# Optimization experiments

Measured on AMD Instinct MI355X. Metric: run time of the kernel, lower is better.

## Reference

```python
import jax, jax.numpy as jnp
import numpy as np

IN_DIM = 128
OUT_DIM = 128
D_MODEL = IN_DIM // 4        # mamba d_model = 32
D_STATE = 16
D_CONV = 4
EXPAND = 2
D_INNER = EXPAND * D_MODEL   # 64
DT_RANK = (D_MODEL + 15) // 16  # ceil(d_model/16) = 2
N_MIXERS = 3                 # shared + 2 experts (stacked on leading axis)
B, DD, HH, WW = 2, 16, 16, 16


def setup_inputs() -> dict:
    key = jax.random.key(0)
    ks = jax.random.split(key, 12)
    rn = lambda k, s, sc=0.05: jax.random.normal(k, s, dtype=jnp.float32) * sc
    M = N_MIXERS
    return {
        "x": jax.random.normal(ks[0], (B, IN_DIM, DD, HH, WW), dtype=jnp.float32),
        "dataset_id": jax.random.randint(ks[1], (B,), 0, 2),
        "ln_g": jnp.ones((M, IN_DIM), jnp.float32),
        "ln_b": jnp.zeros((M, IN_DIM), jnp.float32),
        "in_w": rn(ks[2], (M, 2 * D_INNER, D_MODEL)),
        "conv_w": rn(ks[3], (M, D_INNER, D_CONV), 0.2),
        "conv_b": rn(ks[4], (M, D_INNER), 0.1),
        "xp_w": rn(ks[5], (M, DT_RANK + 2 * D_STATE, D_INNER)),
        "dt_w": rn(ks[6], (M, D_INNER, DT_RANK), 0.2),
        "dt_b": rn(ks[7], (M, D_INNER), 0.1),
        "A_log": jnp.broadcast_to(jnp.log(jnp.arange(1, D_STATE + 1, dtype=jnp.float32)), (M, D_INNER, D_STATE)) + jnp.zeros((M, D_INNER, D_STATE), jnp.float32),
        "Dp": jnp.ones((M, D_INNER), jnp.float32),
        "out_w": rn(ks[8], (M, D_MODEL, D_INNER)),
        "proj_w": rn(ks[9], (M, OUT_DIM, IN_DIM)),
        "proj_b": jnp.zeros((M, OUT_DIM), jnp.float32),
        "skip": jnp.ones((M,), jnp.float32),
    }


def layernorm(x, g, b, eps=1e-5):
    mu = jnp.mean(x, -1, keepdims=True)
    var = jnp.mean((x - mu) ** 2, -1, keepdims=True)
    return (x - mu) * jax.lax.rsqrt(var + eps) * g + b


def mamba(xp, p):
    # Standard Mamba block: in_proj -> causal depthwise conv1d -> selective scan -> SiLU gate -> out_proj
    # xp: (B, L, d_model)
    Bb, L, _ = xp.shape
    xz = jnp.einsum('bld,ed->ble', xp, p["in_w"])            # (B,L,2*d_inner)
    xi, z = jnp.split(xz, 2, axis=-1)
    conv = jax.lax.conv_general_dilated(xi.transpose(0, 2, 1), p["conv_w"][:, None, :], (1,), [(D_CONV - 1, 0)], feature_group_count=D_INNER)
    xi = jax.nn.silu(conv + p["conv_b"][None, :, None]).transpose(0, 2, 1)  # (B,L,d_inner)
    dbc = jnp.einsum('bld,ed->ble', xi, p["xp_w"])
    dt_low = dbc[..., :DT_RANK]
    Bm = dbc[..., DT_RANK:DT_RANK + D_STATE]
    Cm = dbc[..., DT_RANK + D_STATE:]
    delta = jax.nn.softplus(jnp.einsum('blr,dr->bld', dt_low, p["dt_w"]) + p["dt_b"])  # (B,L,d_inner)
    A = -jnp.exp(p["A_log"])                                  # (d_inner, d_state)

    def step(h, inp):
        xt, dt, Bt, Ct = inp                                  # (B,di),(B,di),(B,ds),(B,ds)
        dA = jnp.exp(dt[..., None] * A)                       # (B,d_inner,d_state)
        h = dA * h + (dt * xt)[..., None] * Bt[:, None, :]
        return h, jnp.einsum('bds,bs->bd', h, Ct)

    h0 = jnp.zeros((Bb, D_INNER, D_STATE), xp.dtype)
    xs = (xi.transpose(1, 0, 2), delta.transpose(1, 0, 2), Bm.transpose(1, 0, 2), Cm.transpose(1, 0, 2))
    _, ys = jax.lax.scan(step, h0, xs)
    y = ys.transpose(1, 0, 2) + p["Dp"] * xi
    y = y * jax.nn.silu(z)
    return jnp.einsum('ble,de->bld', y, p["out_w"])


def mixer(x, p):
    # PetaloMixer pom_module='full': LN -> 4-way channel chunk -> shared Mamba + skip -> concat -> LN -> Linear
    Bb, C, Dd, Hh, Ww = x.shape
    L = Dd * Hh * Ww
    xf = x.reshape(Bb, C, L).transpose(0, 2, 1)               # (B,L,C)
    xn = layernorm(xf, p["ln_g"], p["ln_b"])
    parts = jnp.stack(jnp.split(xn, 4, axis=-1), 0)           # (4,B,L,d_model)
    outs = jax.vmap(lambda q: mamba(q, p))(parts) + p["skip"] * parts
    xm = jnp.concatenate([outs[i] for i in range(4)], -1)     # (B,L,C)
    xm = layernorm(xm, p["ln_g"], p["ln_b"])                  # same LayerNorm reused, as in torch code
    xpj = jnp.einsum('blc,oc->blo', xm, p["proj_w"]) + p["proj_b"]
    return xpj.transpose(0, 2, 1).reshape(Bb, OUT_DIM, Dd, Hh, Ww)


def _forward(x, dataset_id, params):
    shared = mixer(x, {k: v[0] for k, v in params.items()})
    # experts: compute both over full batch (vectorized), then per-sample select by dataset_id
    eouts = jax.vmap(lambda p: mixer(x, p))({k: v[1:] for k, v in params.items()})  # (2,B,out,D,H,W)
    ids = jnp.minimum(dataset_id, N_MIXERS - 2)               # clamp: min(m, n_experts-1)
    expert_out = eouts[ids, jnp.arange(x.shape[0])]
    return shared + expert_out                                # Dropout3d(p=0.2) is identity in eval mode


def reference(x, dataset_id, ln_g, ln_b, in_w, conv_w, conv_b, xp_w, dt_w, dt_b, A_log, Dp, out_w, proj_w, proj_b, skip):
    params = dict(ln_g=ln_g, ln_b=ln_b, in_w=in_w, conv_w=conv_w, conv_b=conv_b, xp_w=xp_w, dt_w=dt_w, dt_b=dt_b, A_log=A_log, Dp=Dp, out_w=out_w, proj_w=proj_w, proj_b=proj_b, skip=skip)
    return _forward(x, dataset_id, params)
```

## Files before the change

### kernel.cpp

```cpp
#include <hip/hip_runtime.h>
#include <math.h>

#define LSEQ 4096
#define CIN  128
#define DI   64
#define NS   16
#define NP   4
#define NJ   4
#define NSEQ 16
#define NC   128
#define LC   32
#define LOG2E 1.44269504f
#define LN2   0.6931471806f

__device__ __forceinline__ int mixer_of(const int* did, int j){
  if((j&1)==0) return 0;
  int d = did[j>>1];
  return 1 + (d < 1 ? d : 1);
}
__device__ __forceinline__ float fexp2(float x){ return __builtin_amdgcn_exp2f(x); }
__device__ __forceinline__ float silu_f(float x){
  return x*__builtin_amdgcn_rcpf(1.f + fexp2(-x*LOG2E));
}
__device__ __forceinline__ float softplus_f(float x){
  return x>20.f ? x : LN2*__builtin_amdgcn_logf(1.f + fexp2(x*LOG2E));
}

__global__ __launch_bounds__(256) void k1_ln_inproj(
  const float* __restrict__ x, const int* __restrict__ did,
  const float* __restrict__ ln_g, const float* __restrict__ ln_b,
  const float* __restrict__ in_w,
  float* __restrict__ xnb, float* __restrict__ xzr, float* __restrict__ zb)
{
  const int j = blockIdx.y, b = j>>1, t = threadIdx.x;
  const int l0 = blockIdx.x*16;
  const int m = mixer_of(did, j);
  __shared__ float s_xn[16][132];
  __shared__ float s_mu[16], s_rs[16];

  #pragma unroll
  for(int rep=0; rep<2; rep++){
    int fidx = t + rep*256;
    int c = fidx>>2, fq = fidx&3;
    float4 v = *(const float4*)(x + ((size_t)b*CIN+c)*LSEQ + l0 + fq*4);
    s_xn[fq*4+0][c]=v.x; s_xn[fq*4+1][c]=v.y; s_xn[fq*4+2][c]=v.z; s_xn[fq*4+3][c]=v.w;
  }
  float wreg[32];
  {
    const float4* wp = (const float4*)(in_w + (size_t)m*4096 + (size_t)(t&127)*32);
    #pragma unroll
    for(int i=0;i<8;i++){
      float4 v = wp[i];
      wreg[i*4+0]=v.x; wreg[i*4+1]=v.y; wreg[i*4+2]=v.z; wreg[i*4+3]=v.w;
    }
  }
  __syncthreads();

  {
    const int wv = t>>6, lane = t&63;
    if(wv < 2){
      const int lw = lane&7, g = lane>>3;
      const int ll = wv*8 + lw;
      const float4* xr4 = (const float4*)(&s_xn[ll][g*16]);
      float sum=0.f, vs=0.f;
      #pragma unroll
      for(int k=0;k<4;k++){
        float4 v = xr4[k];
        sum += (v.x+v.y)+(v.z+v.w);
        vs  += v.x*v.x + v.y*v.y + v.z*v.z + v.w*v.w;
      }
      sum += __shfl_xor(sum,8);  vs += __shfl_xor(vs,8);
      sum += __shfl_xor(sum,16); vs += __shfl_xor(vs,16);
      sum += __shfl_xor(sum,32); vs += __shfl_xor(vs,32);
      float mu  = sum*(1.f/128.f);
      float var = fmaxf(vs*(1.f/128.f) - mu*mu, 0.f);
      if(g==0){ s_mu[ll]=mu; s_rs[ll]=rsqrtf(var+1e-5f); }
    }
  }
  __syncthreads();

  #pragma unroll
  for(int rep=0; rep<8; rep++){
    int idx = t + rep*256;
    int ll = idx>>7, c = idx&127;
    float xn = (s_xn[ll][c]-s_mu[ll])*s_rs[ll]*ln_g[m*128+c] + ln_b[m*128+c];
    s_xn[ll][c] = xn;
    xnb[((size_t)j*LSEQ + l0+ll)*128 + c] = xn;
  }
  __syncthreads();

  const int e = t&127, hh = t>>7;
  for(int ll=hh*8; ll<hh*8+8; ++ll){
    #pragma unroll
    for(int q=0;q<4;q++){
      const float4* xr4 = (const float4*)(&s_xn[ll][q*32]);
      float acc=0.f;
      #pragma unroll
      for(int k4=0;k4<8;k4++){
        float4 xv = xr4[k4];
        acc += xv.x*wreg[k4*4+0] + xv.y*wreg[k4*4+1]
             + xv.z*wreg[k4*4+2] + xv.w*wreg[k4*4+3];
      }
      size_t base = ((size_t)(j*NP+q)*LSEQ + l0+ll)*64;
      if(e<64) xzr[base+e]=acc; else zb[base+e-64]=acc;
    }
  }
}

__global__ __launch_bounds__(256) void k2_conv_xproj_pe(
  const int* __restrict__ did,
  const float* __restrict__ conv_w, const float* __restrict__ conv_b,
  const float* __restrict__ xp_w, const float* __restrict__ dt_w, const float* __restrict__ dt_b,
  const float* __restrict__ A_log,
  const float* __restrict__ xzr, float* __restrict__ dxb,
  float* __restrict__ bmb, float* __restrict__ cmb,
  float* __restrict__ pb, float* __restrict__ eb)
{
  const int seq = blockIdx.y, j = seq>>2, t = threadIdx.x;
  const int chunk = blockIdx.x;
  const int l0 = chunk*32;
  const int m = mixer_of(did, j);
  const int d = t&63, r = t>>6;
  __shared__ float  s_xi[32][64];
  __shared__ float  s_dl[32][64];
  __shared__ float  s_bS[32][16];
  __shared__ float  s_dbc[32][2];
  __shared__ float  s_cwT[4][64];
  __shared__ float  s_xpw01[2][64];
  __shared__ float  s_cb[64], s_dtw[128], s_dtb[64];

  float lz[11];
  #pragma unroll
  for(int i=0;i<11;i++){
    int l = l0 + r*8 - 3 + i;
    lz[i] = (l>=0) ? xzr[((size_t)seq*LSEQ + l)*64 + d] : 0.f;
  }
  { int k=t>>6, dd=t&63; s_cwT[k][dd]=conv_w[m*256+dd*4+k]; }
  if(t<64){ s_cb[t]=conv_b[m*64+t]; s_dtb[t]=dt_b[m*64+t]; }
  if(t<128){ s_dtw[t]=dt_w[m*128+t]; s_xpw01[t>>6][t&63]=xp_w[m*2176 + t]; }
  const int o2 = t&31, rg = t>>5;
  float wreg[64];
  {
    const float4* wp = (const float4*)(xp_w + (size_t)m*2176 + (size_t)(2+o2)*64);
    #pragma unroll
    for(int k4=0;k4<16;k4++){
      float4 v = wp[k4];
      wreg[k4*4+0]=v.x; wreg[k4*4+1]=v.y; wreg[k4*4+2]=v.z; wreg[k4*4+3]=v.w;
    }
  }
  __syncthreads();

  float xir[8];
  {
    float cw0=s_cwT[0][d], cw1=s_cwT[1][d], cw2=s_cwT[2][d], cw3=s_cwT[3][d], cb=s_cb[d];
    #pragma unroll
    for(int i=0;i<8;i++){
      float xc = cb + lz[i]*cw0 + lz[i+1]*cw1 + lz[i+2]*cw2 + lz[i+3]*cw3;
      xir[i] = silu_f(xc);
      s_xi[r*8+i][d] = xir[i];
    }
  }

  {
    float pr[8];
    #pragma unroll
    for(int i=0;i<8;i++){
      float p0 = xir[i]*s_xpw01[0][d];
      float p1 = xir[i]*s_xpw01[1][d];
      float q0 = p0 + __shfl_xor(p0,1);
      float q1 = p1 + __shfl_xor(p1,1);
      pr[i] = (d&1) ? q1 : q0;
    }
    #pragma unroll
    for(int off=2; off<64; off<<=1){
      #pragma unroll
      for(int i=0;i<8;i++) pr[i] += __shfl_xor(pr[i], off);
    }
    if(d<2){
      #pragma unroll
      for(int i=0;i<8;i++) s_dbc[r*8+i][d] = pr[i];
    }
  }
  __syncthreads();

  {
    float w0=s_dtw[d*2], w1=s_dtw[d*2+1], bb=s_dtb[d];
    #pragma unroll
    for(int i=0;i<8;i++){
      int ll=r*8+i;
      float dtv = s_dbc[ll][0]*w0 + s_dbc[ll][1]*w1 + bb;
      float dlv = softplus_f(dtv);
      s_dl[ll][d] = dlv;
      *(float2*)(dxb + ((size_t)seq*LSEQ + l0+ll)*128 + d*2) = make_float2(dlv, xir[i]);
    }
  }

  {
    #pragma unroll
    for(int ip=0; ip<2; ip++){
      int ll = rg*4 + ip*2;
      const float4* xa=(const float4*)&s_xi[ll][0];
      const float4* xb=(const float4*)&s_xi[ll+1][0];
      float a0=0.f,a1=0.f,b0=0.f,b1=0.f;
      #pragma unroll
      for(int k=0;k<16;k+=2){
        float4 u=xa[k], u2=xa[k+1], v=xb[k], v2=xb[k+1];
        a0 += u.x *wreg[4*k+0]+u.y *wreg[4*k+1]+u.z *wreg[4*k+2]+u.w *wreg[4*k+3];
        a1 += u2.x*wreg[4*k+4]+u2.y*wreg[4*k+5]+u2.z*wreg[4*k+6]+u2.w*wreg[4*k+7];
        b0 += v.x *wreg[4*k+0]+v.y *wreg[4*k+1]+v.z *wreg[4*k+2]+v.w *wreg[4*k+3];
        b1 += v2.x*wreg[4*k+4]+v2.y*wreg[4*k+5]+v2.z*wreg[4*k+6]+v2.w*wreg[4*k+7];
      }
      float A=a0+a1, Bv=b0+b1;
      if(o2<16){
        s_bS[ll][o2]=A; s_bS[ll+1][o2]=Bv;
        bmb[((size_t)seq*LSEQ + l0+ll  )*16 + o2]=A;
        bmb[((size_t)seq*LSEQ + l0+ll+1)*16 + o2]=Bv;
      } else {
        cmb[((size_t)seq*LSEQ + l0+ll  )*16 + o2-16]=A;
        cmb[((size_t)seq*LSEQ + l0+ll+1)*16 + o2-16]=Bv;
      }
    }
  }
  __syncthreads();

  {
    const int sq = r;
    float as_q[4], as0;
    {
      const float* ap = A_log + (size_t)m*1024 + d*16;
      as0 = -expf(ap[0])*LOG2E;
      #pragma unroll
      for(int k=0;k<4;k++) as_q[k] = -expf(ap[sq*4+k])*LOG2E;
    }
    bool stl = true;
    #pragma unroll
    for(int k=0;k<4;k++){ float ex=(float)(sq*4+k+1)*as0; stl = stl && (fabsf(as_q[k]-ex) <= 1e-4f*fabsf(ex)); }
    const bool structured = (__ballot(stl) == ~0ull);

    float E[4] = {0.f,0.f,0.f,0.f};
    float Sdl = 0.f;

    #define PSTEPF(i_, P0CODE) { \
      float dl = s_dl[i_][d]; \
      float u  = dl * s_xi[i_][d]; \
      Sdl += dl; \
      const float4 bv = *(const float4*)(&s_bS[i_][sq*4]); \
      float q = fexp2(dl*as0); \
      float q2 = q*q; float q4 = q2*q2; (void)q2; (void)q4; \
      float p0 = (P0CODE); \
      float p1 = p0*q, p2 = p1*q, p3 = p2*q; \
      E[0]=fmaf(p0,E[0],u*bv.x); E[1]=fmaf(p1,E[1],u*bv.y); \
      E[2]=fmaf(p2,E[2],u*bv.z); E[3]=fmaf(p3,E[3],u*bv.w); }

    #define PSTEPG(i_) { \
      float dl = s_dl[i_][d]; \
      float u  = dl * s_xi[i_][d]; \
      Sdl += dl; \
      const float4 bv = *(const float4*)(&s_bS[i_][sq*4]); \
      float p_[4]; \
      _Pragma("unroll") for(int k=0;k<4;k++) p_[k]=fexp2(dl*as_q[k]); \
      E[0]=fmaf(p_[0],E[0],u*bv.x); E[1]=fmaf(p_[1],E[1],u*bv.y); \
      E[2]=fmaf(p_[2],E[2],u*bv.z); E[3]=fmaf(p_[3],E[3],u*bv.w); }

    if(structured){
      if(sq==0){
        #pragma unroll 4
        for(int i=0;i<LC;i++){ PSTEPF(i, q) }
      } else if(sq==1){
        #pragma unroll 4
        for(int i=0;i<LC;i++){ PSTEPF(i, q4*q) }
      } else if(sq==2){
        #pragma unroll 4
        for(int i=0;i<LC;i++){ PSTEPF(i, (q4*q4)*q) }
      } else {
        #pragma unroll 4
        for(int i=0;i<LC;i++){ PSTEPF(i, ((q4*q4)*q4)*q) }
      }
    } else {
      #pragma unroll 4
      for(int i=0;i<LC;i++){ PSTEPG(i) }
    }
    #undef PSTEPF
    #undef PSTEPG

    size_t oo=(((size_t)seq*NC+chunk)*64+d)*16 + sq*4;
    *(float4*)(pb+oo) = make_float4(fexp2(Sdl*as_q[0]),fexp2(Sdl*as_q[1]),
                                    fexp2(Sdl*as_q[2]),fexp2(Sdl*as_q[3]));
    *(float4*)(eb+oo) = make_float4(E[0],E[1],E[2],E[3]);
  }
}

__global__ __launch_bounds__(256) void k3b_combine(
  float* p_hs, const float* __restrict__ eb)
{
  const int seq=blockIdx.y, q=blockIdx.x, t=threadIdx.x;
  const size_t elem = (size_t)q*256+t;
  #define OFF(c_) (((size_t)seq*NC+(c_))*1024 + elem)
  float pA[16],eA[16],pB[16],eB[16];
  #pragma unroll
  for(int k=0;k<16;k++){ pA[k]=p_hs[OFF(k)]; eA[k]=eb[OFF(k)]; }
  float h=0.f;
  for(int bt=0; bt<8; bt+=2){
    if(bt+1<8){
      #pragma unroll
      for(int k=0;k<16;k++){ pB[k]=p_hs[OFF((bt+1)*16+k)]; eB[k]=eb[OFF((bt+1)*16+k)]; }
    }
    #pragma unroll
    for(int k=0;k<16;k++){ p_hs[OFF(bt*16+k)]=h; h=fmaf(pA[k],h,eA[k]); }
    if(bt+2<8){
      #pragma unroll
      for(int k=0;k<16;k++){ pA[k]=p_hs[OFF((bt+2)*16+k)]; eA[k]=eb[OFF((bt+2)*16+k)]; }
    }
    #pragma unroll
    for(int k=0;k<16;k++){ p_hs[OFF((bt+1)*16+k)]=h; h=fmaf(pB[k],h,eB[k]); }
  }
  #undef OFF
}

__global__ __launch_bounds__(256) void k3c4_scan_outproj(
  const int* __restrict__ did, const float* __restrict__ A_log, const float* __restrict__ Dp,
  const float* __restrict__ dxb,
  const float* __restrict__ bmb, const float* __restrict__ cmb,
  const float* __restrict__ zb, const float* __restrict__ hsb,
  const float* __restrict__ out_w, const float* __restrict__ skipv,
  const float* __restrict__ xnb, float* __restrict__ xmb)
{
  const int seq=blockIdx.y, j=seq>>2, p=seq&3, t=threadIdx.x;
  const int wave=t>>6, d=t&63;
  const int cl=wave>>1, sh=wave&1, sh8=sh*8;
  const int chunk=blockIdx.x*2+cl;
  const int l0=blockIdx.x*2*LC;
  const int m=mixer_of(did,j);
  __shared__ float s_b[2*LC*NS];
  __shared__ float s_c[2*LC*NS];
  __shared__ float s_y0[64*64];
  __shared__ float s_y1[64*64];
  {
    const float4* bsrc=(const float4*)(bmb + ((size_t)seq*LSEQ + l0)*NS);
    const float4* csrc=(const float4*)(cmb + ((size_t)seq*LSEQ + l0)*NS);
    ((float4*)s_b)[t]=bsrc[t];
    ((float4*)s_c)[t]=csrc[t];
  }
  float as_h[8], as0;
  {
    const float* ap = A_log + (size_t)m*1024 + d*16;
    as0 = -expf(ap[0])*LOG2E;
    #pragma unroll
    for(int k=0;k<8;k++) as_h[k] = -expf(ap[sh8+k])*LOG2E;
  }
  bool stl = true;
  #pragma unroll
  for(int k=0;k<8;k++){ float ex=(float)(sh8+k+1)*as0; stl = stl && (fabsf(as_h[k]-ex) <= 1e-4f*fabsf(ex)); }
  const bool structured = (__ballot(stl) == ~0ull);

  const float dpv2 = (sh==0) ? Dp[m*64+d] : 0.f;
  float h[8];
  {
    const float4* hp=(const float4*)(hsb + (((size_t)seq*NC+chunk)*64+d)*16 + sh8);
    float4 v0=hp[0], v1=hp[1];
    h[0]=v0.x; h[1]=v0.y; h[2]=v0.z; h[3]=v0.w;
    h[4]=v1.x; h[5]=v1.y; h[6]=v1.z; h[7]=v1.w;
  }
  const float2* dxp=(const float2*)(dxb + ((size_t)seq*LSEQ + (size_t)chunk*LC)*128);
  float* s_yw = sh ? s_y1 : s_y0;
  __syncthreads();

  #define CSTEPF(i_, dx_, P0CODE) { \
    float dl=dx_.x, xv=dx_.y; float u=dl*xv; \
    const float4* bq=(const float4*)(s_b + cl*(LC*NS) + (i_)*NS + sh8); \
    const float4* cq=(const float4*)(s_c + cl*(LC*NS) + (i_)*NS + sh8); \
    float4 b0=bq[0],b1=bq[1],c0=cq[0],c1=cq[1]; \
    float bb[8]={b0.x,b0.y,b0.z,b0.w, b1.x,b1.y,b1.z,b1.w}; \
    float cc2[8]={c0.x,c0.y,c0.z,c0.w, c1.x,c1.y,c1.z,c1.w}; \
    float q=fexp2(dl*as0); \
    float q2=q*q; float q4=q2*q2; (void)q2; (void)q4; \
    float pz[8]; pz[0]=(P0CODE); \
    _Pragma("unroll") for(int k=1;k<8;k++) pz[k]=pz[k-1]*q; \
    float ya=0.f, yb2=0.f; \
    _Pragma("unroll") for(int k=0;k<8;k++){ \
      h[k]=fmaf(pz[k],h[k],u*bb[k]); \
      float hv=h[k]*cc2[k]; \
      if(k&1) yb2+=hv; else ya+=hv; } \
    float y=ya+yb2; y=fmaf(dpv2,xv,y); \
    s_yw[(cl*LC+(i_))*64 + d]=y; }

  #define CSTEPG(i_, dx_) { \
    float dl=dx_.x, xv=dx_.y; float u=dl*xv; \
    const float4* bq=(const float4*)(s_b + cl*(LC*NS) + (i_)*NS + sh8); \
    const float4* cq=(const float4*)(s_c + cl*(LC*NS) + (i_)*NS + sh8); \
    float4 b0=bq[0],b1=bq[1],c0=cq[0],c1=cq[1]; \
    float bb[8]={b0.x,b0.y,b0.z,b0.w, b1.x,b1.y,b1.z,b1.w}; \
    float cc2[8]={c0.x,c0.y,c0.z,c0.w, c1.x,c1.y,c1.z,c1.w}; \
    float pz[8]; \
    _Pragma("unroll") for(int k=0;k<8;k++) pz[k]=fexp2(dl*as_h[k]); \
    float ya=0.f, yb2=0.f; \
    _Pragma("unroll") for(int k=0;k<8;k++){ \
      h[k]=fmaf(pz[k],h[k],u*bb[k]); \
      float hv=h[k]*cc2[k]; \
      if(k&1) yb2+=hv; else ya+=hv; } \
    float y=ya+yb2; y=fmaf(dpv2,xv,y); \
    s_yw[(cl*LC+(i_))*64 + d]=y; }

  #define CLOOPF(P0CODE) { \
    float2 dxw[4]; \
    _Pragma("unroll") for(int k=0;k<4;k++) dxw[k]=dxp[k*64+d]; \
    for(int ii=0;ii<LC;ii+=4){ \
      float2 c0w=dxw[0],c1w=dxw[1],c2w=dxw[2],c3w=dxw[3]; \
      if(ii+4<LC){ _Pragma("unroll") for(int k=0;k<4;k++) dxw[k]=dxp[(ii+4+k)*64+d]; } \
      CSTEPF(ii+0,c0w,P0CODE); CSTEPF(ii+1,c1w,P0CODE); \
      CSTEPF(ii+2,c2w,P0CODE); CSTEPF(ii+3,c3w,P0CODE); } }

  if(structured){
    if(sh==0){ CLOOPF(q) }
    else     { CLOOPF((q4*q4)*q) }
  } else {
    float2 dxw[4];
    #pragma unroll
    for(int k=0;k<4;k++) dxw[k]=dxp[k*64+d];
    for(int ii=0;ii<LC;ii+=4){
      float2 c0w=dxw[0],c1w=dxw[1],c2w=dxw[2],c3w=dxw[3];
      if(ii+4<LC){
        #pragma unroll
        for(int k=0;k<4;k++) dxw[k]=dxp[(ii+4+k)*64+d];
      }
      CSTEPG(ii+0,c0w); CSTEPG(ii+1,c1w); CSTEPG(ii+2,c2w); CSTEPG(ii+3,c3w);
    }
  }
  #undef CLOOPF
  #undef CSTEPF
  #undef CSTEPG

  __syncthreads();
  {
    const float* zp = zb + ((size_t)seq*LSEQ + l0)*64;
    #pragma unroll
    for(int it=0; it<16; ++it){
      int idx = t + it*256;
      float ysum = s_y0[idx] + s_y1[idx];
      s_y0[idx] = ysum * silu_f(zp[idx]);
    }
  }
  const int o=t&31, grp=t>>5;
  float wreg[64];
  {
    const float4* wp=(const float4*)(out_w + (size_t)m*2048 + (size_t)o*64);
    #pragma unroll
    for(int k4=0;k4<16;k4++){
      float4 v=wp[k4];
      wreg[k4*4+0]=v.x; wreg[k4*4+1]=v.y; wreg[k4*4+2]=v.z; wreg[k4*4+3]=v.w;
    }
  }
  const float sk=skipv[m];
  __syncthreads();
  for(int ll=grp; ll<64; ll+=8){
    const float4* ya=(const float4*)&s_y0[ll*64];
    float a0=0.f,a1=0.f;
    #pragma unroll
    for(int k=0;k<16;k+=2){
      float4 u=ya[k], u2=ya[k+1];
      a0 += u.x *wreg[4*k+0]+u.y *wreg[4*k+1]+u.z *wreg[4*k+2]+u.w *wreg[4*k+3];
      a1 += u2.x*wreg[4*k+4]+u2.y*wreg[4*k+5]+u2.z*wreg[4*k+6]+u2.w*wreg[4*k+7];
    }
    size_t xidx=((size_t)j*LSEQ + l0+ll)*128 + p*32 + o;
    xmb[xidx]=(a0+a1) + sk*xnb[xidx];
  }
}

__global__ __launch_bounds__(256) void k5_ln2_proj(
  const int* __restrict__ did, const float* __restrict__ ln_g, const float* __restrict__ ln_b,
  const float* __restrict__ proj_w, const float* __restrict__ proj_b,
  const float* __restrict__ xmb, float* __restrict__ out)
{
  const int b=blockIdx.y, l0=blockIdx.x*8, t=threadIdx.x;
  const int eh = t>>7, local = t&127;
  const int j = 2*b+eh;
  const int m = mixer_of(did, j);
  __shared__ float s_xn[2][8][132];
  __shared__ float s_comb[8][132];
  __shared__ float s_murs[2][8][2];

  for(int idx=local; idx<1024; idx+=128){
    int ll=idx>>7, c=idx&127;
    s_xn[eh][ll][c] = xmb[((size_t)j*LSEQ + l0+ll)*128 + c];
  }
  __syncthreads();
  if(((t>>6)&1)==0){
    const int lane = t&63;
    const int g = lane&7, ll = lane>>3;
    float sum=0.f, vs=0.f;
    const float4* xr4 = (const float4*)(&s_xn[eh][ll][g*16]);
    #pragma unroll
    for(int k=0;k<4;k++){
      float4 v = xr4[k];
      sum += (v.x+v.y)+(v.z+v.w);
      vs  += v.x*v.x + v.y*v.y + v.z*v.z + v.w*v.w;
    }
    sum += __shfl_xor(sum,1); vs += __shfl_xor(vs,1);
    sum += __shfl_xor(sum,2); vs += __shfl_xor(vs,2);
    sum += __shfl_xor(sum,4); vs += __shfl_xor(vs,4);
    float mu  = sum*(1.f/128.f);
    float var = fmaxf(vs*(1.f/128.f) - mu*mu, 0.f);
    if(g==0){ s_murs[eh][ll][0]=mu; s_murs[eh][ll][1]=rsqrtf(var+1e-5f); }
  }
  __syncthreads();
  for(int idx=local; idx<1024; idx+=128){
    int ll=idx>>7, c=idx&127;
    float xn=(s_xn[eh][ll][c]-s_murs[eh][ll][0])*s_murs[eh][ll][1]*ln_g[m*128+c]+ln_b[m*128+c];
    s_xn[eh][ll][c]=xn;
  }
  __syncthreads();
  float acc[8];
  #pragma unroll
  for(int ll=0;ll<8;ll++) acc[ll]=0.f;
  {
    const float4* pw4 = (const float4*)(proj_w + (size_t)m*16384 + (size_t)local*128);
    #pragma unroll 4
    for(int c4=0;c4<32;c4++){
      float4 w = pw4[c4];
      int c = c4*4;
      #pragma unroll
      for(int ll=0;ll<8;ll++){
        acc[ll] += w.x*s_xn[eh][ll][c] + w.y*s_xn[eh][ll][c+1]
                 + w.z*s_xn[eh][ll][c+2] + w.w*s_xn[eh][ll][c+3];
      }
    }
  }
  float pb_v = proj_b[m*128+local];
  if(eh==0){
    #pragma unroll
    for(int ll=0;ll<8;ll++) s_comb[ll][local]=acc[ll]+pb_v;
  }
  __syncthreads();
  if(eh==1){
    #pragma unroll
    for(int ll=0;ll<8;ll++) s_comb[ll][local]+=acc[ll]+pb_v;
  }
  __syncthreads();
  for(int idx=t; idx<1024; idx+=256){
    int o=idx>>3, ll=idx&7;
    out[((size_t)b*128+o)*LSEQ + l0+ll] = s_comb[ll][o];
  }
}

extern "C" void kernel_launch(void* const* d_in, const int* in_sizes, int n_in,
                              void* d_out, int out_size, void* d_ws, size_t ws_size,
                              hipStream_t stream) {
  const float* x      = (const float*)d_in[0];
  const int*   did    = (const int*)d_in[1];
  const float* ln_g   = (const float*)d_in[2];
  const float* ln_b   = (const float*)d_in[3];
  const float* in_w   = (const float*)d_in[4];
  const float* conv_w = (const float*)d_in[5];
  const float* conv_b = (const float*)d_in[6];
  const float* xp_w   = (const float*)d_in[7];
  const float* dt_w   = (const float*)d_in[8];
  const float* dt_b   = (const float*)d_in[9];
  const float* A_log  = (const float*)d_in[10];
  const float* Dp     = (const float*)d_in[11];
  const float* out_w  = (const float*)d_in[12];
  const float* proj_w = (const float*)d_in[13];
  const float* proj_b = (const float*)d_in[14];
  const float* skipv  = (const float*)d_in[15];
  float* out = (float*)d_out;
  float* ws  = (float*)d_ws;

  float* xnb = ws;
  float* xzr = xnb + (size_t)NJ*LSEQ*128;
  float* zb  = xzr + (size_t)NSEQ*LSEQ*64;
  float* dxb = zb  + (size_t)NSEQ*LSEQ*64;
  float* bmb = dxb + (size_t)NSEQ*LSEQ*128;
  float* cmb = bmb + (size_t)NSEQ*LSEQ*16;
  float* xmb = cmb + (size_t)NSEQ*LSEQ*16;
  float* pb  = xmb + (size_t)NJ*LSEQ*128;
  float* eb  = pb  + (size_t)NSEQ*NC*1024;
  float* hsb = pb;

  hipLaunchKernelGGL(k1_ln_inproj, dim3(LSEQ/16,NJ), dim3(256), 0, stream,
                     x,did,ln_g,ln_b,in_w,xnb,xzr,zb);
  hipLaunchKernelGGL(k2_conv_xproj_pe, dim3(NC,NSEQ), dim3(256), 0, stream,
                     did,conv_w,conv_b,xp_w,dt_w,dt_b,A_log,xzr,dxb,bmb,cmb,pb,eb);
  hipLaunchKernelGGL(k3b_combine, dim3(4,NSEQ), dim3(256), 0, stream, pb,eb);
  hipLaunchKernelGGL(k3c4_scan_outproj, dim3(NC/2,NSEQ), dim3(256), 0, stream,
                     did,A_log,Dp,dxb,bmb,cmb,zb,hsb,out_w,skipv,xnb,xmb);
  hipLaunchKernelGGL(k5_ln2_proj, dim3(LSEQ/8,2), dim3(256), 0, stream,
                     did,ln_g,ln_b,proj_w,proj_b,xmb,out);
}
```

Measured before the change: 119.4 us.

## Fuse LayerNorm/in-projection kernel into conv/x-projection kernel with halo recompute

```diff
diff --git a/kernel.cpp b/kernel.cpp
--- a/kernel.cpp
+++ b/kernel.cpp
@@ -26,42 +26,64 @@
   return x>20.f ? x : LN2*__builtin_amdgcn_logf(1.f + fexp2(x*LOG2E));
 }
 
-__global__ __launch_bounds__(256) void k1_ln_inproj(
+__global__ __launch_bounds__(256) void k12_fused(
   const float* __restrict__ x, const int* __restrict__ did,
   const float* __restrict__ ln_g, const float* __restrict__ ln_b,
   const float* __restrict__ in_w,
-  float* __restrict__ xnb, float* __restrict__ xzr, float* __restrict__ zb)
+  const float* __restrict__ conv_w, const float* __restrict__ conv_b,
+  const float* __restrict__ xp_w, const float* __restrict__ dt_w, const float* __restrict__ dt_b,
+  const float* __restrict__ A_log,
+  float* __restrict__ xnb, float* __restrict__ zb, float* __restrict__ dxb,
+  float* __restrict__ bmb, float* __restrict__ cmb,
+  float* __restrict__ pb, float* __restrict__ eb)
 {
-  const int j = blockIdx.y, b = j>>1, t = threadIdx.x;
-  const int l0 = blockIdx.x*16;
+  const int seq = blockIdx.y, j = seq>>2, q = seq&3, b = j>>1;
+  const int chunk = blockIdx.x, l0 = chunk*32;
   const int m = mixer_of(did, j);
-  __shared__ float s_xn[16][132];
-  __shared__ float s_mu[16], s_rs[16];
-
-  #pragma unroll
-  for(int rep=0; rep<2; rep++){
-    int fidx = t + rep*256;
-    int c = fidx>>2, fq = fidx&3;
-    float4 v = *(const float4*)(x + ((size_t)b*CIN+c)*LSEQ + l0 + fq*4);
-    s_xn[fq*4+0][c]=v.x; s_xn[fq*4+1][c]=v.y; s_xn[fq*4+2][c]=v.z; s_xn[fq*4+3][c]=v.w;
-  }
-  float wreg[32];
+  const int t = threadIdx.x, d = t&63, r = t>>6;
+
+  __shared__ float s_x[36*132];
+  __shared__ float s_xn[36][36];
+  __shared__ float s_xzf[35][64];
+  __shared__ float s_bS[32][16];
+  __shared__ float s_dbc[32][2];
+  __shared__ float s_cwT[4][64];
+  __shared__ float s_xpw01[2][64];
+  __shared__ float s_cb[64], s_dtw[128], s_dtb[64];
+  __shared__ float s_mu[36], s_rs[36];
+  float* s_xi = s_x;
+  float* s_dl = s_x + 2048;
+
+  for(int idx=t; idx<1152; idx+=256){
+    int c = idx/9, f = idx - c*9;
+    int l = l0 - 4 + f*4;
+    float4 v;
+    if(l >= 0) v = *(const float4*)(x + ((size_t)b*CIN + c)*LSEQ + l);
+    else       v = make_float4(0.f,0.f,0.f,0.f);
+    s_x[(f*4+0)*132 + c] = v.x;
+    s_x[(f*4+1)*132 + c] = v.y;
+    s_x[(f*4+2)*132 + c] = v.z;
+    s_x[(f*4+3)*132 + c] = v.w;
+  }
+  float wreg_in[32];
   {
     const float4* wp = (const float4*)(in_w + (size_t)m*4096 + (size_t)(t&127)*32);
     #pragma unroll
     for(int i=0;i<8;i++){
       float4 v = wp[i];
-      wreg[i*4+0]=v.x; wreg[i*4+1]=v.y; wreg[i*4+2]=v.z; wreg[i*4+3]=v.w;
-    }
-  }
-  __syncthreads();
-
-  {
-    const int wv = t>>6, lane = t&63;
-    if(wv < 2){
-      const int lw = lane&7, g = lane>>3;
-      const int ll = wv*8 + lw;
-      const float4* xr4 = (const float4*)(&s_xn[ll][g*16]);
+      wreg_in[i*4+0]=v.x; wreg_in[i*4+1]=v.y; wreg_in[i*4+2]=v.z; wreg_in[i*4+3]=v.w;
+    }
+  }
+  { int k=t>>6, dd=t&63; s_cwT[k][dd]=conv_w[m*256+dd*4+k]; }
+  if(t<64){ s_cb[t]=conv_b[m*64+t]; s_dtb[t]=dt_b[m*64+t]; }
+  if(t<128){ s_dtw[t]=dt_w[m*128+t]; s_xpw01[t>>6][t&63]=xp_w[m*2176 + t]; }
+  __syncthreads();
+
+  {
+    const int lane=t&63, g=lane&7, lw=lane>>3;
+    {
+      int row = r*8 + lw;
+      const float4* xr4 = (const float4*)(s_x + row*132 + g*16);
       float sum=0.f, vs=0.f;
       #pragma unroll
       for(int k=0;k<4;k++){
@@ -69,75 +91,73 @@
         sum += (v.x+v.y)+(v.z+v.w);
         vs  += v.x*v.x + v.y*v.y + v.z*v.z + v.w*v.w;
       }
-      sum += __shfl_xor(sum,8);  vs += __shfl_xor(vs,8);
-      sum += __shfl_xor(sum,16); vs += __shfl_xor(vs,16);
-      sum += __shfl_xor(sum,32); vs += __shfl_xor(vs,32);
+      sum += __shfl_xor(sum,1); vs += __shfl_xor(vs,1);
+      sum += __shfl_xor(sum,2); vs += __shfl_xor(vs,2);
+      sum += __shfl_xor(sum,4); vs += __shfl_xor(vs,4);
       float mu  = sum*(1.f/128.f);
       float var = fmaxf(vs*(1.f/128.f) - mu*mu, 0.f);
-      if(g==0){ s_mu[ll]=mu; s_rs[ll]=rsqrtf(var+1e-5f); }
-    }
-  }
-  __syncthreads();
-
-  #pragma unroll
-  for(int rep=0; rep<8; rep++){
-    int idx = t + rep*256;
-    int ll = idx>>7, c = idx&127;
-    float xn = (s_xn[ll][c]-s_mu[ll])*s_rs[ll]*ln_g[m*128+c] + ln_b[m*128+c];
-    s_xn[ll][c] = xn;
-    xnb[((size_t)j*LSEQ + l0+ll)*128 + c] = xn;
-  }
-  __syncthreads();
-
-  const int e = t&127, hh = t>>7;
-  for(int ll=hh*8; ll<hh*8+8; ++ll){
-    #pragma unroll
-    for(int q=0;q<4;q++){
-      const float4* xr4 = (const float4*)(&s_xn[ll][q*32]);
-      float acc=0.f;
-      #pragma unroll
-      for(int k4=0;k4<8;k4++){
-        float4 xv = xr4[k4];
-        acc += xv.x*wreg[k4*4+0] + xv.y*wreg[k4*4+1]
-             + xv.z*wreg[k4*4+2] + xv.w*wreg[k4*4+3];
-      }
-      size_t base = ((size_t)(j*NP+q)*LSEQ + l0+ll)*64;
-      if(e<64) xzr[base+e]=acc; else zb[base+e-64]=acc;
-    }
-  }
-}
-
-__global__ __launch_bounds__(256) void k2_conv_xproj_pe(
-  const int* __restrict__ did,
-  const float* __restrict__ conv_w, const float* __restrict__ conv_b,
-  const float* __restrict__ xp_w, const float* __restrict__ dt_w, const float* __restrict__ dt_b,
-  const float* __restrict__ A_log,
-  const float* __restrict__ xzr, float* __restrict__ dxb,
-  float* __restrict__ bmb, float* __restrict__ cmb,
-  float* __restrict__ pb, float* __restrict__ eb)
-{
-  const int seq = blockIdx.y, j = seq>>2, t = threadIdx.x;
-  const int chunk = blockIdx.x;
-  const int l0 = chunk*32;
-  const int m = mixer_of(did, j);
-  const int d = t&63, r = t>>6;
-  __shared__ float  s_xi[32][64];
-  __shared__ float  s_dl[32][64];
-  __shared__ float  s_bS[32][16];
-  __shared__ float  s_dbc[32][2];
-  __shared__ float  s_cwT[4][64];
-  __shared__ float  s_xpw01[2][64];
-  __shared__ float  s_cb[64], s_dtw[128], s_dtb[64];
-
-  float lz[11];
-  #pragma unroll
-  for(int i=0;i<11;i++){
-    int l = l0 + r*8 - 3 + i;
-    lz[i] = (l>=0) ? xzr[((size_t)seq*LSEQ + l)*64 + d] : 0.f;
-  }
-  { int k=t>>6, dd=t&63; s_cwT[k][dd]=conv_w[m*256+dd*4+k]; }
-  if(t<64){ s_cb[t]=conv_b[m*64+t]; s_dtb[t]=dt_b[m*64+t]; }
-  if(t<128){ s_dtw[t]=dt_w[m*128+t]; s_xpw01[t>>6][t&63]=xp_w[m*2176 + t]; }
+      if(g==0){ s_mu[row]=mu; s_rs[row]=rsqrtf(var+1e-5f); }
+    }
+    if(r==0 && lw<4){
+      int row = 32 + lw;
+      const float4* xr4 = (const float4*)(s_x + row*132 + g*16);
+      float sum=0.f, vs=0.f;
+      #pragma unroll
+      for(int k=0;k<4;k++){
+        float4 v = xr4[k];
+        sum += (v.x+v.y)+(v.z+v.w);
+        vs  += v.x*v.x + v.y*v.y + v.z*v.z + v.w*v.w;
+      }
+      sum += __shfl_xor(sum,1); vs += __shfl_xor(vs,1);
+      sum += __shfl_xor(sum,2); vs += __shfl_xor(vs,2);
+      sum += __shfl_xor(sum,4); vs += __shfl_xor(vs,4);
+      float mu  = sum*(1.f/128.f);
+      float var = fmaxf(vs*(1.f/128.f) - mu*mu, 0.f);
+      if(g==0){ s_mu[row]=mu; s_rs[row]=rsqrtf(var+1e-5f); }
+    }
+  }
+  __syncthreads();
+
+  for(int idx=t; idx<1120; idx+=256){
+    int row = (idx>>5) + 1, cc = idx&31;
+    float xv = s_x[row*132 + q*32 + cc];
+    float xn = (xv - s_mu[row])*s_rs[row]*ln_g[m*128 + q*32+cc] + ln_b[m*128 + q*32+cc];
+    s_xn[row][cc] = xn;
+    if(row>=4) xnb[((size_t)j*LSEQ + l0+row-4)*128 + q*32+cc] = xn;
+  }
+  __syncthreads();
+
+  {
+    const int e = t&127, hh = t>>7;
+    if(e < 64){
+      int r0 = 1 + hh*18, r1 = hh ? 36 : 19;
+      for(int row=r0; row<r1; ++row){
+        const float4* xr4 = (const float4*)(&s_xn[row][0]);
+        float acc=0.f;
+        #pragma unroll
+        for(int k4=0;k4<8;k4++){
+          float4 xv = xr4[k4];
+          acc += xv.x*wreg_in[k4*4+0] + xv.y*wreg_in[k4*4+1]
+               + xv.z*wreg_in[k4*4+2] + xv.w*wreg_in[k4*4+3];
+        }
+        if(chunk==0 && row<4) acc = 0.f;
+        s_xzf[row-1][e] = acc;
+      }
+    } else {
+      int r0 = 4 + hh*16, r1 = r0 + 16;
+      for(int row=r0; row<r1; ++row){
+        const float4* xr4 = (const float4*)(&s_xn[row][0]);
+        float acc=0.f;
+        #pragma unroll
+        for(int k4=0;k4<8;k4++){
+          float4 xv = xr4[k4];
+          acc += xv.x*wreg_in[k4*4+0] + xv.y*wreg_in[k4*4+1]
+               + xv.z*wreg_in[k4*4+2] + xv.w*wreg_in[k4*4+3];
+        }
+        zb[((size_t)seq*LSEQ + l0+row-4)*64 + (e-64)] = acc;
+      }
+    }
+  }
   const int o2 = t&31, rg = t>>5;
   float wreg[64];
   {
@@ -152,12 +172,15 @@
 
   float xir[8];
   {
+    float lz[11];
+    #pragma unroll
+    for(int i=0;i<11;i++) lz[i] = s_xzf[r*8+i][d];
     float cw0=s_cwT[0][d], cw1=s_cwT[1][d], cw2=s_cwT[2][d], cw3=s_cwT[3][d], cb=s_cb[d];
     #pragma unroll
     for(int i=0;i<8;i++){
       float xc = cb + lz[i]*cw0 + lz[i+1]*cw1 + lz[i+2]*cw2 + lz[i+3]*cw3;
       xir[i] = silu_f(xc);
-      s_xi[r*8+i][d] = xir[i];
+      s_xi[(r*8+i)*64 + d] = xir[i];
     }
   }
 
@@ -190,7 +213,7 @@
       int ll=r*8+i;
       float dtv = s_dbc[ll][0]*w0 + s_dbc[ll][1]*w1 + bb;
       float dlv = softplus_f(dtv);
-      s_dl[ll][d] = dlv;
+      s_dl[ll*64 + d] = dlv;
       *(float2*)(dxb + ((size_t)seq*LSEQ + l0+ll)*128 + d*2) = make_float2(dlv, xir[i]);
     }
   }
@@ -199,8 +222,8 @@
     #pragma unroll
     for(int ip=0; ip<2; ip++){
       int ll = rg*4 + ip*2;
-      const float4* xa=(const float4*)&s_xi[ll][0];
-      const float4* xb=(const float4*)&s_xi[ll+1][0];
+      const float4* xa=(const float4*)(s_xi + ll*64);
+      const float4* xb=(const float4*)(s_xi + (ll+1)*64);
       float a0=0.f,a1=0.f,b0=0.f,b1=0.f;
       #pragma unroll
       for(int k=0;k<16;k+=2){
@@ -241,20 +264,20 @@
     float Sdl = 0.f;
 
     #define PSTEPF(i_, P0CODE) { \
-      float dl = s_dl[i_][d]; \
-      float u  = dl * s_xi[i_][d]; \
+      float dl = s_dl[(i_)*64 + d]; \
+      float u  = dl * s_xi[(i_)*64 + d]; \
       Sdl += dl; \
       const float4 bv = *(const float4*)(&s_bS[i_][sq*4]); \
-      float q = fexp2(dl*as0); \
-      float q2 = q*q; float q4 = q2*q2; (void)q2; (void)q4; \
+      float qv = fexp2(dl*as0); \
+      float q2 = qv*qv; float q4 = q2*q2; (void)q2; (void)q4; \
       float p0 = (P0CODE); \
-      float p1 = p0*q, p2 = p1*q, p3 = p2*q; \
+      float p1 = p0*qv, p2 = p1*qv, p3 = p2*qv; \
       E[0]=fmaf(p0,E[0],u*bv.x); E[1]=fmaf(p1,E[1],u*bv.y); \
       E[2]=fmaf(p2,E[2],u*bv.z); E[3]=fmaf(p3,E[3],u*bv.w); }
 
     #define PSTEPG(i_) { \
-      float dl = s_dl[i_][d]; \
-      float u  = dl * s_xi[i_][d]; \
+      float dl = s_dl[(i_)*64 + d]; \
+      float u  = dl * s_xi[(i_)*64 + d]; \
       Sdl += dl; \
       const float4 bv = *(const float4*)(&s_bS[i_][sq*4]); \
       float p_[4]; \
@@ -265,16 +288,16 @@
     if(structured){
       if(sq==0){
         #pragma unroll 4
-        for(int i=0;i<LC;i++){ PSTEPF(i, q) }
+        for(int i=0;i<LC;i++){ PSTEPF(i, qv) }
       } else if(sq==1){
         #pragma unroll 4
-        for(int i=0;i<LC;i++){ PSTEPF(i, q4*q) }
+        for(int i=0;i<LC;i++){ PSTEPF(i, q4*qv) }
       } else if(sq==2){
         #pragma unroll 4
-        for(int i=0;i<LC;i++){ PSTEPF(i, (q4*q4)*q) }
+        for(int i=0;i<LC;i++){ PSTEPF(i, (q4*q4)*qv) }
       } else {
         #pragma unroll 4
-        for(int i=0;i<LC;i++){ PSTEPF(i, ((q4*q4)*q4)*q) }
+        for(int i=0;i<LC;i++){ PSTEPF(i, ((q4*q4)*q4)*qv) }
       }
     } else {
       #pragma unroll 4
@@ -372,10 +395,10 @@
     float4 b0=bq[0],b1=bq[1],c0=cq[0],c1=cq[1]; \
     float bb[8]={b0.x,b0.y,b0.z,b0.w, b1.x,b1.y,b1.z,b1.w}; \
     float cc2[8]={c0.x,c0.y,c0.z,c0.w, c1.x,c1.y,c1.z,c1.w}; \
-    float q=fexp2(dl*as0); \
-    float q2=q*q; float q4=q2*q2; (void)q2; (void)q4; \
+    float qv=fexp2(dl*as0); \
+    float q2=qv*qv; float q4=q2*q2; (void)q2; (void)q4; \
     float pz[8]; pz[0]=(P0CODE); \
-    _Pragma("unroll") for(int k=1;k<8;k++) pz[k]=pz[k-1]*q; \
+    _Pragma("unroll") for(int k=1;k<8;k++) pz[k]=pz[k-1]*qv; \
     float ya=0.f, yb2=0.f; \
     _Pragma("unroll") for(int k=0;k<8;k++){ \
       h[k]=fmaf(pz[k],h[k],u*bb[k]); \
@@ -411,8 +434,8 @@
       CSTEPF(ii+2,c2w,P0CODE); CSTEPF(ii+3,c3w,P0CODE); } }
 
   if(structured){
-    if(sh==0){ CLOOPF(q) }
-    else     { CLOOPF((q4*q4)*q) }
+    if(sh==0){ CLOOPF(qv) }
+    else     { CLOOPF((q4*q4)*qv) }
   } else {
     float2 dxw[4];
     #pragma unroll
@@ -565,8 +588,7 @@
   float* ws  = (float*)d_ws;
 
   float* xnb = ws;
-  float* xzr = xnb + (size_t)NJ*LSEQ*128;
-  float* zb  = xzr + (size_t)NSEQ*LSEQ*64;
+  float* zb  = xnb + (size_t)NJ*LSEQ*128;
   float* dxb = zb  + (size_t)NSEQ*LSEQ*64;
   float* bmb = dxb + (size_t)NSEQ*LSEQ*128;
   float* cmb = bmb + (size_t)NSEQ*LSEQ*16;
@@ -575,10 +597,9 @@
   float* eb  = pb  + (size_t)NSEQ*NC*1024;
   float* hsb = pb;
 
-  hipLaunchKernelGGL(k1_ln_inproj, dim3(LSEQ/16,NJ), dim3(256), 0, stream,
-                     x,did,ln_g,ln_b,in_w,xnb,xzr,zb);
-  hipLaunchKernelGGL(k2_conv_xproj_pe, dim3(NC,NSEQ), dim3(256), 0, stream,
-                     did,conv_w,conv_b,xp_w,dt_w,dt_b,A_log,xzr,dxb,bmb,cmb,pb,eb);
+  hipLaunchKernelGGL(k12_fused, dim3(NC,NSEQ), dim3(256), 0, stream,
+                     x,did,ln_g,ln_b,in_w,conv_w,conv_b,xp_w,dt_w,dt_b,A_log,
+                     xnb,zb,dxb,bmb,cmb,pb,eb);
   hipLaunchKernelGGL(k3b_combine, dim3(4,NSEQ), dim3(256), 0, stream, pb,eb);
   hipLaunchKernelGGL(k3c4_scan_outproj, dim3(NC/2,NSEQ), dim3(256), 0, stream,
                      did,A_log,Dp,dxb,bmb,cmb,zb,hsb,out_w,skipv,xnb,xmb);
```

After: 119.1 us (median of 3 runs). About the same (-0.2%).
